# Kernel optimization log

Hardware: AMD Instinct MI355X
Metric: run time of the kernel (lower is better)

## Reference

```python
import jax, jax.numpy as jnp
import numpy as np

N_NODES = 100000
N_EDGES = 1200000
D_IN = 64
D_HID = 64
D_OUT = 32


def setup_inputs() -> dict:
    key = jax.random.key(0)
    ks = jax.random.split(key, 8)
    x = jax.random.normal(ks[0], (N_NODES, D_IN), dtype=jnp.float32)
    edge_index = jax.random.randint(ks[1], (2, N_EDGES), 0, N_NODES, dtype=jnp.int64)
    s = 0.05
    W1 = jax.random.normal(ks[2], (D_IN, D_HID), dtype=jnp.float32) * s
    b1 = jnp.zeros((D_HID,), dtype=jnp.float32)
    W2 = jax.random.normal(ks[3], (D_HID, D_HID), dtype=jnp.float32) * s
    b2 = jnp.zeros((D_HID,), dtype=jnp.float32)
    Wl = jax.random.normal(ks[4], (D_HID, D_OUT), dtype=jnp.float32) * s
    bl = jax.random.normal(ks[5], (D_OUT,), dtype=jnp.float32) * s
    return {"x": x, "edge_index": edge_index, "W1": W1, "b1": b1,
            "W2": W2, "b2": b2, "Wl": Wl, "bl": bl}


def reference(x, edge_index, W1, b1, W2, b2, Wl, bl):
    n = x.shape[0]
    # PyG GCNConv default: add self-loops, symmetric normalization D^-1/2 (A+I) D^-1/2
    loops = jnp.arange(n, dtype=edge_index.dtype)
    src = jnp.concatenate([edge_index[0], loops])  # message sources
    dst = jnp.concatenate([edge_index[1], loops])  # aggregation targets
    deg = jax.ops.segment_sum(jnp.ones(dst.shape, x.dtype), dst, num_segments=n)
    dinv = jax.lax.rsqrt(deg)  # deg >= 1 due to self-loops
    norm = dinv[src] * dinv[dst]  # [E+N]

    def gcn_conv(h, W, b):
        h = h @ W                      # transform [N, d]
        m = h[src] * norm[:, None]     # gather + scale [E+N, d]
        return jax.ops.segment_sum(m, dst, num_segments=n) + b  # scatter-add

    h = jax.nn.relu(gcn_conv(x, W1, b1))
    h = jax.nn.relu(gcn_conv(h, W2, b2))
    return h @ Wl + bl
```

## Files before the change

kernel.cpp:

```cpp
#include <hip/hip_runtime.h>
#include <hip/hip_fp16.h>

#define N_NODES 100000
#define N_EDGES 1200000

#define BIN_SHIFT 6
#define NODES_PER_BIN 64
#define NBINS ((N_NODES + NODES_PER_BIN - 1) >> BIN_SHIFT)
#define CAP 1024
#define EPB 8192
#define NBLK_BIN ((N_EDGES + EPB - 1) / EPB)

__global__ void binning_kernel(const int* __restrict__ src, const int* __restrict__ dst,
                               int* __restrict__ gcursor, unsigned int* __restrict__ binned,
                               int E) {
    __shared__ unsigned int stage[EPB];
    __shared__ unsigned short sbin[EPB];
    __shared__ unsigned int hist[NBINS];
    int t = threadIdx.x;
    int e_base = blockIdx.x * EPB;

    for (int b = t; b < NBINS; b += 256) hist[b] = 0;
    __syncthreads();

#pragma unroll
    for (int j = 0; j < EPB / 256; ++j) {
        int idx = e_base + t + j * 256;
        if (idx < E) {
            int s = src[idx];
            int d = dst[idx];
            unsigned int bin = (unsigned int)d >> BIN_SHIFT;
            stage[t + j * 256] = (unsigned int)s | (((unsigned int)d & 63u) << 17);
            sbin[t + j * 256] = (unsigned short)bin;
            atomicAdd(&hist[bin], 1u);
        }
    }
    __syncthreads();

    for (int b = t; b < NBINS; b += 256) {
        unsigned int c = hist[b];
        if (c) hist[b] = (unsigned int)(b * CAP) + (unsigned int)atomicAdd(&gcursor[b], (int)c);
    }
    __syncthreads();

#pragma unroll
    for (int j = 0; j < EPB / 256; ++j) {
        int idx = e_base + t + j * 256;
        if (idx < E) {
            unsigned int bin = sbin[t + j * 256];
            unsigned int pos = atomicAdd(&hist[bin], 1u);
            binned[pos] = stage[t + j * 256];
        }
    }
}

__global__ void csr_kernel(unsigned int* __restrict__ binned,
                           const int* __restrict__ gcursor,
                           float* __restrict__ dinv,
                           unsigned int* __restrict__ offdeg) {
    __shared__ unsigned int eLDS[CAP];
    __shared__ unsigned int counts[NODES_PER_BIN];
    __shared__ unsigned int scan[NODES_PER_BIN];
    __shared__ unsigned int offs[NODES_PER_BIN];
    __shared__ unsigned int cur[NODES_PER_BIN];
    int bin = blockIdx.x;
    int t = threadIdx.x;
    int nb = gcursor[bin];
    unsigned int* eb = binned + (size_t)bin * CAP;

    if (t < NODES_PER_BIN) counts[t] = 0;
    __syncthreads();
    for (int i = t; i < nb; i += 256) {
        unsigned int p = eb[i];
        eLDS[i] = p;
        atomicAdd(&counts[p >> 17], 1u);
    }
    __syncthreads();
    if (t < NODES_PER_BIN) scan[t] = counts[t];
    __syncthreads();
    for (int step = 1; step < NODES_PER_BIN; step <<= 1) {
        unsigned int v = 0;
        if (t < NODES_PER_BIN && t >= step) v = scan[t - step];
        __syncthreads();
        if (t < NODES_PER_BIN) scan[t] += v;
        __syncthreads();
    }
    if (t < NODES_PER_BIN) {
        offs[t] = scan[t] - counts[t];
        cur[t] = 0;
    }
    __syncthreads();
    for (int i = t; i < nb; i += 256) {
        unsigned int p = eLDS[i];
        unsigned int l = p >> 17;
        unsigned int pos = offs[l] + atomicAdd(&cur[l], 1u);
        eb[pos] = p & 0x1FFFFu;
    }
    if (t < NODES_PER_BIN) {
        int node = bin * NODES_PER_BIN + t;
        if (node < N_NODES) {
            dinv[node] = rsqrtf((float)(counts[t] + 1u));
            offdeg[node] = (offs[t] << 16) | counts[t];
        }
    }
}

template<int DOUT, bool HALF_OUT>
__global__ __launch_bounds__(256, 4) void gemm_kernel(const float* __restrict__ X,
                                                      const float* __restrict__ W,
                                                      const float* __restrict__ bias,
                                                      const float* __restrict__ rowscale,
                                                      void* __restrict__ Hout, int n) {
    constexpr int COLG = DOUT / 4;
    constexpr int RGS  = 256 / COLG;
    constexpr int RPT  = 64 / RGS;
    constexpr int XPITCH = 17;
    __shared__ float4 sW4[64 * COLG];
    __shared__ float4 sX4[64 * XPITCH];
    int tid = threadIdx.x;

    for (int i = tid; i < 64 * COLG; i += 256) sW4[i] = ((const float4*)W)[i];

    int base_row = blockIdx.x * 64;
    const float4* X4 = (const float4*)X;
    for (int i = tid; i < 64 * 16; i += 256) {
        int r = i >> 4, c = i & 15;
        int gr = base_row + r;
        float4 v = make_float4(0.f, 0.f, 0.f, 0.f);
        if (gr < n) v = X4[(size_t)gr * 16 + c];
        sX4[r * XPITCH + c] = v;
    }
    __syncthreads();

    int cg = tid % COLG;
    int rg = tid / COLG;
    float4 acc[RPT];
#pragma unroll
    for (int r = 0; r < RPT; ++r) acc[r] = make_float4(0.f, 0.f, 0.f, 0.f);

#pragma unroll 2
    for (int k4 = 0; k4 < 16; ++k4) {
        float4 xv[RPT];
#pragma unroll
        for (int r = 0; r < RPT; ++r) xv[r] = sX4[(rg + RGS * r) * XPITCH + k4];
#pragma unroll
        for (int kk = 0; kk < 4; ++kk) {
            float4 w = sW4[(k4 * 4 + kk) * COLG + cg];
#pragma unroll
            for (int r = 0; r < RPT; ++r) {
                float xs = (kk == 0) ? xv[r].x : (kk == 1) ? xv[r].y : (kk == 2) ? xv[r].z : xv[r].w;
                acc[r].x = fmaf(xs, w.x, acc[r].x);
                acc[r].y = fmaf(xs, w.y, acc[r].y);
                acc[r].z = fmaf(xs, w.z, acc[r].z);
                acc[r].w = fmaf(xs, w.w, acc[r].w);
            }
        }
    }

#pragma unroll
    for (int r = 0; r < RPT; ++r) {
        int grow = base_row + rg + RGS * r;
        if (grow < n) {
            float4 v = acc[r];
            if (rowscale) {
                float s = rowscale[grow];
                v.x *= s; v.y *= s; v.z *= s; v.w *= s;
            }
            if (bias) {
                float4 bb = ((const float4*)bias)[cg];
                v.x += bb.x; v.y += bb.y; v.z += bb.z; v.w += bb.w;
            }
            if (HALF_OUT) {
                __half2* H2 = (__half2*)Hout;
                size_t idx = (size_t)grow * (DOUT / 2) + 2 * cg;
                H2[idx]     = __floats2half2_rn(v.x, v.y);
                H2[idx + 1] = __floats2half2_rn(v.z, v.w);
            } else {
                ((float4*)Hout)[(size_t)grow * COLG + cg] = v;
            }
        }
    }
}

__global__ void aggregate_kernel(const __half* __restrict__ tmp,
                                 const unsigned int* __restrict__ binned,
                                 const int* __restrict__ gcursor,
                                 const unsigned int* __restrict__ offdeg,
                                 const float* __restrict__ dinv,
                                 const float* __restrict__ b,
                                 float* __restrict__ h) {
    __shared__ unsigned int srcs[CAP];
    __shared__ unsigned int sOffdeg[NODES_PER_BIN];
    __shared__ float sDinv[NODES_PER_BIN];
    int bin = blockIdx.x;
    int t = threadIdx.x;
    int nb = gcursor[bin];
    const unsigned int* eb = binned + (size_t)bin * CAP;

    if (t < NODES_PER_BIN) {
        int node = bin * NODES_PER_BIN + t;
        sOffdeg[t] = (node < N_NODES) ? offdeg[node] : 0;
        sDinv[t] = (node < N_NODES) ? dinv[node] : 0.0f;
    }
    for (int i = t; i < nb; i += 256) srcs[i] = eb[i];
    __syncthreads();

    int oct = t & 7;
    int lnode0 = t >> 3;
    const uint4* tmp16 = (const uint4*)tmp;
    float bb[8];
    {
        const float4 b0 = ((const float4*)b)[oct * 2];
        const float4 b1 = ((const float4*)b)[oct * 2 + 1];
        bb[0] = b0.x; bb[1] = b0.y; bb[2] = b0.z; bb[3] = b0.w;
        bb[4] = b1.x; bb[5] = b1.y; bb[6] = b1.z; bb[7] = b1.w;
    }

#pragma unroll
    for (int g = 0; g < 2; ++g) {
        int ln = g * 32 + lnode0;
        int node = bin * NODES_PER_BIN + ln;
        if (node < N_NODES) {
            unsigned int od = sOffdeg[ln];
            int deg = (int)(od & 0xFFFFu);
            int beg = (int)(od >> 16);
            float acc[8];
            {
                uint4 raw = tmp16[(size_t)node * 8 + oct];
                const __half2* hp = (const __half2*)&raw;
#pragma unroll
                for (int j = 0; j < 4; ++j) {
                    float2 f = __half22float2(hp[j]);
                    acc[2 * j] = f.x; acc[2 * j + 1] = f.y;
                }
            }
            int e = 0;
            for (; e + 3 < deg; e += 4) {
                unsigned int s0 = srcs[beg + e];
                unsigned int s1 = srcs[beg + e + 1];
                unsigned int s2 = srcs[beg + e + 2];
                unsigned int s3 = srcs[beg + e + 3];
                uint4 r0 = tmp16[(size_t)s0 * 8 + oct];
                uint4 r1 = tmp16[(size_t)s1 * 8 + oct];
                uint4 r2 = tmp16[(size_t)s2 * 8 + oct];
                uint4 r3 = tmp16[(size_t)s3 * 8 + oct];
                const __half2* h0 = (const __half2*)&r0;
                const __half2* h1 = (const __half2*)&r1;
                const __half2* h2 = (const __half2*)&r2;
                const __half2* h3 = (const __half2*)&r3;
#pragma unroll
                for (int j = 0; j < 4; ++j) {
                    float2 f0 = __half22float2(h0[j]);
                    float2 f1 = __half22float2(h1[j]);
                    float2 f2 = __half22float2(h2[j]);
                    float2 f3 = __half22float2(h3[j]);
                    acc[2 * j]     += (f0.x + f1.x) + (f2.x + f3.x);
                    acc[2 * j + 1] += (f0.y + f1.y) + (f2.y + f3.y);
                }
            }
            for (; e < deg; ++e) {
                unsigned int s0 = srcs[beg + e];
                uint4 r0 = tmp16[(size_t)s0 * 8 + oct];
                const __half2* h0 = (const __half2*)&r0;
#pragma unroll
                for (int j = 0; j < 4; ++j) {
                    float2 f0 = __half22float2(h0[j]);
                    acc[2 * j]     += f0.x;
                    acc[2 * j + 1] += f0.y;
                }
            }
            float dv = sDinv[ln];
            float4 o0, o1;
            o0.x = fmaxf(fmaf(dv, acc[0], bb[0]), 0.0f);
            o0.y = fmaxf(fmaf(dv, acc[1], bb[1]), 0.0f);
            o0.z = fmaxf(fmaf(dv, acc[2], bb[2]), 0.0f);
            o0.w = fmaxf(fmaf(dv, acc[3], bb[3]), 0.0f);
            o1.x = fmaxf(fmaf(dv, acc[4], bb[4]), 0.0f);
            o1.y = fmaxf(fmaf(dv, acc[5], bb[5]), 0.0f);
            o1.z = fmaxf(fmaf(dv, acc[6], bb[6]), 0.0f);
            o1.w = fmaxf(fmaf(dv, acc[7], bb[7]), 0.0f);
            float4* hv = (float4*)(h + (size_t)node * 64 + oct * 8);
            hv[0] = o0;
            hv[1] = o1;
        }
    }
}

extern "C" void kernel_launch(void* const* d_in, const int* in_sizes, int n_in,
                              void* d_out, int out_size, void* d_ws, size_t ws_size,
                              hipStream_t stream) {
    const float* x  = (const float*)d_in[0];
    const int*   ei = (const int*)d_in[1];
    const float* W1 = (const float*)d_in[2];
    const float* b1 = (const float*)d_in[3];
    const float* W2 = (const float*)d_in[4];
    const float* b2 = (const float*)d_in[5];
    const float* Wl = (const float*)d_in[6];
    const float* bl = (const float*)d_in[7];
    float* out = (float*)d_out;

    const int N = N_NODES;
    const int E = N_EDGES;
    const int* src = ei;
    const int* dst = ei + E;

    char* ws = (char*)d_ws;
    size_t off = 0;
    auto align = [](size_t v) { return (v + 511) & ~(size_t)511; };
    int* gcursor         = (int*)(ws + off);          off = align(off + (size_t)NBINS * 4);
    float* dinv          = (float*)(ws + off);        off = align(off + (size_t)N * 4);
    unsigned int* offdeg = (unsigned int*)(ws + off); off = align(off + (size_t)N * 4);
    unsigned int* binned = (unsigned int*)(ws + off); off = align(off + (size_t)NBINS * CAP * 4);
    __half* tmp          = (__half*)(ws + off);       off = align(off + (size_t)N * 64 * 2);
    float* h             = (float*)(ws + off);        off = align(off + (size_t)N * 64 * 4);
    (void)ws_size;

    const int NBLK_GEMM = (N + 63) / 64;

    hipMemsetAsync(gcursor, 0, (size_t)NBINS * 4, stream);
    binning_kernel<<<NBLK_BIN, 256, 0, stream>>>(src, dst, gcursor, binned, E);
    csr_kernel<<<NBINS, 256, 0, stream>>>(binned, gcursor, dinv, offdeg);

    gemm_kernel<64, true><<<NBLK_GEMM, 256, 0, stream>>>(x, W1, nullptr, dinv, tmp, N);
    aggregate_kernel<<<NBINS, 256, 0, stream>>>(tmp, binned, gcursor, offdeg, dinv, b1, h);

    gemm_kernel<64, true><<<NBLK_GEMM, 256, 0, stream>>>(h, W2, nullptr, dinv, tmp, N);
    aggregate_kernel<<<NBINS, 256, 0, stream>>>(tmp, binned, gcursor, offdeg, b2 ? dinv : dinv, b2, h);

    gemm_kernel<32, false><<<NBLK_GEMM, 256, 0, stream>>>(h, Wl, bl, nullptr, out, N);
}
```

Baseline: 219.9 us.

## Fuse aggregation with following dense transform per node bin

The aggregate kernel now keeps its ReLU'd 64-wide output for each 64-node bin in shared memory and immediately multiplies it by the next weight matrix (W2 or Wl) inside the same block. This removes two gemm launches and the fp32 round trip of the hidden activations through global memory. The intermediate is now written as half precision (tmp2) instead of fp32. In exchange it raises shared memory use per block, which may lower occupancy, and adds a second block-wide sync.

New measurement: 204.5 us. 7.0% less time.

```diff
diff --git a/kernel.cpp b/kernel.cpp
--- a/kernel.cpp
+++ b/kernel.cpp
@@ -105,15 +105,13 @@
     }
 }
 
-template<int DOUT, bool HALF_OUT>
-__global__ __launch_bounds__(256, 4) void gemm_kernel(const float* __restrict__ X,
-                                                      const float* __restrict__ W,
-                                                      const float* __restrict__ bias,
-                                                      const float* __restrict__ rowscale,
-                                                      void* __restrict__ Hout, int n) {
-    constexpr int COLG = DOUT / 4;
-    constexpr int RGS  = 256 / COLG;
-    constexpr int RPT  = 64 / RGS;
+__global__ __launch_bounds__(256, 4) void gemm1_kernel(const float* __restrict__ X,
+                                                       const float* __restrict__ W,
+                                                       const float* __restrict__ rowscale,
+                                                       __half* __restrict__ Hout, int n) {
+    constexpr int COLG = 16;
+    constexpr int RGS  = 16;
+    constexpr int RPT  = 4;
     constexpr int XPITCH = 17;
     __shared__ float4 sW4[64 * COLG];
     __shared__ float4 sX4[64 * XPITCH];
@@ -162,45 +160,47 @@
         int grow = base_row + rg + RGS * r;
         if (grow < n) {
             float4 v = acc[r];
-            if (rowscale) {
-                float s = rowscale[grow];
-                v.x *= s; v.y *= s; v.z *= s; v.w *= s;
-            }
-            if (bias) {
-                float4 bb = ((const float4*)bias)[cg];
-                v.x += bb.x; v.y += bb.y; v.z += bb.z; v.w += bb.w;
-            }
-            if (HALF_OUT) {
-                __half2* H2 = (__half2*)Hout;
-                size_t idx = (size_t)grow * (DOUT / 2) + 2 * cg;
-                H2[idx]     = __floats2half2_rn(v.x, v.y);
-                H2[idx + 1] = __floats2half2_rn(v.z, v.w);
-            } else {
-                ((float4*)Hout)[(size_t)grow * COLG + cg] = v;
-            }
-        }
-    }
-}
-
-__global__ void aggregate_kernel(const __half* __restrict__ tmp,
-                                 const unsigned int* __restrict__ binned,
-                                 const int* __restrict__ gcursor,
-                                 const unsigned int* __restrict__ offdeg,
-                                 const float* __restrict__ dinv,
-                                 const float* __restrict__ b,
-                                 float* __restrict__ h) {
+            float s = rowscale[grow];
+            v.x *= s; v.y *= s; v.z *= s; v.w *= s;
+            __half2* H2 = (__half2*)Hout;
+            size_t idx = (size_t)grow * 32 + 2 * cg;
+            H2[idx]     = __floats2half2_rn(v.x, v.y);
+            H2[idx + 1] = __floats2half2_rn(v.z, v.w);
+        }
+    }
+}
+
+template<int DOUT, bool HALF_OUT, bool ROWSCALE, bool GEMM_BIAS>
+__global__ __launch_bounds__(256, 4) void fused_agg_gemm(
+    const __half* __restrict__ tmp,
+    const unsigned int* __restrict__ binned,
+    const int* __restrict__ gcursor,
+    const unsigned int* __restrict__ offdeg,
+    const float* __restrict__ dinv,
+    const float* __restrict__ gb,
+    const float* __restrict__ W,
+    const float* __restrict__ gbias,
+    void* __restrict__ Hout) {
+    constexpr int COLG = DOUT / 4;
+    constexpr int RGS  = 256 / COLG;
+    constexpr int RPT  = 64 / RGS;
+    constexpr int XPITCH = 17;
     __shared__ unsigned int srcs[CAP];
     __shared__ unsigned int sOffdeg[NODES_PER_BIN];
     __shared__ float sDinv[NODES_PER_BIN];
+    __shared__ float4 sW4[64 * COLG];
+    __shared__ float4 sH4[64 * XPITCH];
+
     int bin = blockIdx.x;
     int t = threadIdx.x;
     int nb = gcursor[bin];
     const unsigned int* eb = binned + (size_t)bin * CAP;
 
+    for (int i = t; i < 64 * COLG; i += 256) sW4[i] = ((const float4*)W)[i];
     if (t < NODES_PER_BIN) {
         int node = bin * NODES_PER_BIN + t;
         sOffdeg[t] = (node < N_NODES) ? offdeg[node] : 0;
-        sDinv[t] = (node < N_NODES) ? dinv[node] : 0.0f;
+        sDinv[t]   = (node < N_NODES) ? dinv[node]   : 0.0f;
     }
     for (int i = t; i < nb; i += 256) srcs[i] = eb[i];
     __syncthreads();
@@ -210,8 +210,8 @@
     const uint4* tmp16 = (const uint4*)tmp;
     float bb[8];
     {
-        const float4 b0 = ((const float4*)b)[oct * 2];
-        const float4 b1 = ((const float4*)b)[oct * 2 + 1];
+        const float4 b0 = ((const float4*)gb)[oct * 2];
+        const float4 b1 = ((const float4*)gb)[oct * 2 + 1];
         bb[0] = b0.x; bb[1] = b0.y; bb[2] = b0.z; bb[3] = b0.w;
         bb[4] = b1.x; bb[5] = b1.y; bb[6] = b1.z; bb[7] = b1.w;
     }
@@ -279,9 +279,59 @@
             o1.y = fmaxf(fmaf(dv, acc[5], bb[5]), 0.0f);
             o1.z = fmaxf(fmaf(dv, acc[6], bb[6]), 0.0f);
             o1.w = fmaxf(fmaf(dv, acc[7], bb[7]), 0.0f);
-            float4* hv = (float4*)(h + (size_t)node * 64 + oct * 8);
-            hv[0] = o0;
-            hv[1] = o1;
+            sH4[ln * XPITCH + oct * 2]     = o0;
+            sH4[ln * XPITCH + oct * 2 + 1] = o1;
+        }
+    }
+    __syncthreads();
+
+    int cg = t % COLG;
+    int rg = t / COLG;
+    float4 acc[RPT];
+#pragma unroll
+    for (int r = 0; r < RPT; ++r) acc[r] = make_float4(0.f, 0.f, 0.f, 0.f);
+
+#pragma unroll 2
+    for (int k4 = 0; k4 < 16; ++k4) {
+        float4 xv[RPT];
+#pragma unroll
+        for (int r = 0; r < RPT; ++r) xv[r] = sH4[(rg + RGS * r) * XPITCH + k4];
+#pragma unroll
+        for (int kk = 0; kk < 4; ++kk) {
+            float4 w = sW4[(k4 * 4 + kk) * COLG + cg];
+#pragma unroll
+            for (int r = 0; r < RPT; ++r) {
+                float xs = (kk == 0) ? xv[r].x : (kk == 1) ? xv[r].y : (kk == 2) ? xv[r].z : xv[r].w;
+                acc[r].x = fmaf(xs, w.x, acc[r].x);
+                acc[r].y = fmaf(xs, w.y, acc[r].y);
+                acc[r].z = fmaf(xs, w.z, acc[r].z);
+                acc[r].w = fmaf(xs, w.w, acc[r].w);
+            }
+        }
+    }
+
+#pragma unroll
+    for (int r = 0; r < RPT; ++r) {
+        int ln = rg + RGS * r;
+        int node = bin * NODES_PER_BIN + ln;
+        if (node < N_NODES) {
+            float4 v = acc[r];
+            if (ROWSCALE) {
+                float s = sDinv[ln];
+                v.x *= s; v.y *= s; v.z *= s; v.w *= s;
+            }
+            if (GEMM_BIAS) {
+                float4 bbq = ((const float4*)gbias)[cg];
+                v.x += bbq.x; v.y += bbq.y; v.z += bbq.z; v.w += bbq.w;
+            }
+            if (HALF_OUT) {
+                __half2* H2 = (__half2*)Hout;
+                size_t idx = (size_t)node * (DOUT / 2) + 2 * cg;
+                H2[idx]     = __floats2half2_rn(v.x, v.y);
+                H2[idx + 1] = __floats2half2_rn(v.z, v.w);
+            } else {
+                ((float4*)Hout)[(size_t)node * COLG + cg] = v;
+            }
         }
     }
 }
@@ -312,7 +362,7 @@
     unsigned int* offdeg = (unsigned int*)(ws + off); off = align(off + (size_t)N * 4);
     unsigned int* binned = (unsigned int*)(ws + off); off = align(off + (size_t)NBINS * CAP * 4);
     __half* tmp          = (__half*)(ws + off);       off = align(off + (size_t)N * 64 * 2);
-    float* h             = (float*)(ws + off);        off = align(off + (size_t)N * 64 * 4);
+    __half* tmp2         = (__half*)(ws + off);       off = align(off + (size_t)N * 64 * 2);
     (void)ws_size;
 
     const int NBLK_GEMM = (N + 63) / 64;
@@ -321,11 +371,11 @@
     binning_kernel<<<NBLK_BIN, 256, 0, stream>>>(src, dst, gcursor, binned, E);
     csr_kernel<<<NBINS, 256, 0, stream>>>(binned, gcursor, dinv, offdeg);
 
-    gemm_kernel<64, true><<<NBLK_GEMM, 256, 0, stream>>>(x, W1, nullptr, dinv, tmp, N);
-    aggregate_kernel<<<NBINS, 256, 0, stream>>>(tmp, binned, gcursor, offdeg, dinv, b1, h);
-
-    gemm_kernel<64, true><<<NBLK_GEMM, 256, 0, stream>>>(h, W2, nullptr, dinv, tmp, N);
-    aggregate_kernel<<<NBINS, 256, 0, stream>>>(tmp, binned, gcursor, offdeg, b2 ? dinv : dinv, b2, h);
-
-    gemm_kernel<32, false><<<NBLK_GEMM, 256, 0, stream>>>(h, Wl, bl, nullptr, out, N);
-}
+    gemm1_kernel<<<NBLK_GEMM, 256, 0, stream>>>(x, W1, dinv, tmp, N);
+
+    fused_agg_gemm<64, true, true, false><<<NBINS, 256, 0, stream>>>(
+        tmp, binned, gcursor, offdeg, dinv, b1, W2, nullptr, tmp2);
+
+    fused_agg_gemm<32, false, false, true><<<NBINS, 256, 0, stream>>>(
+        tmp2, binned, gcursor, offdeg, dinv, b2, Wl, bl, out);
+}
```
